# Kernel tuning notes

Hardware: AMD Instinct MI355X
Metric: run time of the kernel (lower is better)

## Reference

```python
import jax, jax.numpy as jnp
import numpy as np

B, QT, KT = 4, 1024, 1024
Q_SIZE, K_SIZE, EMB, HEADS = 1024, 1024, 1024, 8
HEAD_DIM = EMB // HEADS


def setup_inputs() -> dict:
    key = jax.random.key(0)
    ks = jax.random.split(key, 8)
    query = jax.random.normal(ks[0], (B, QT, Q_SIZE), dtype=jnp.float32)
    key_t = jax.random.normal(ks[1], (B, KT, K_SIZE), dtype=jnp.float32)
    mask = jax.random.randint(ks[2], (B, QT, KT), 0, 2, dtype=jnp.int32)
    # Linear weights stored as (in, out); torch Linear computes x @ W.T, equivalent here.
    sq = 1.0 / np.sqrt(Q_SIZE)
    sk = 1.0 / np.sqrt(K_SIZE)
    se = 1.0 / np.sqrt(EMB)
    Wq = jax.random.uniform(ks[3], (Q_SIZE, EMB), jnp.float32, -sq, sq)
    Wk = jax.random.uniform(ks[4], (K_SIZE, EMB), jnp.float32, -sk, sk)
    Wv = jax.random.uniform(ks[5], (K_SIZE, EMB), jnp.float32, -sk, sk)
    Wu = jax.random.uniform(ks[6], (EMB, EMB), jnp.float32, -se, se)
    bu = jax.random.uniform(ks[7], (EMB,), jnp.float32, -se, se)
    return {"query": query, "key": key_t, "mask": mask,
            "Wq": Wq, "Wk": Wk, "Wv": Wv, "Wu": Wu, "bu": bu}


def reference(query, key, mask, Wq, Wk, Wv, Wu, bu):
    b, q_t, _ = query.shape
    k_t = key.shape[1]
    q = (query @ Wq).reshape(b, q_t, HEADS, HEAD_DIM)   # b i n d
    k = (key @ Wk).reshape(b, k_t, HEADS, HEAD_DIM)     # b j n d
    v = (key @ Wv).reshape(b, k_t, HEADS, HEAD_DIM)
    # NOTE: original module defines self.scale but never applies it.
    att_score = jnp.einsum('bind,bjnd->bijn', q, k)
    att_score = jnp.where(mask[..., None] == 0, jnp.float32(-1e9), att_score)
    att_prob = jax.nn.softmax(att_score, axis=2)        # softmax over key axis j
    att_vec = jnp.einsum('bijn,bjnd->bind', att_prob, v).reshape(b, q_t, EMB)
    return att_vec @ Wu + bu
```

## Files before the change

kernel.cpp:

```cpp
#include <hip/hip_runtime.h>
#include <hip/hip_bf16.h>


typedef __attribute__((ext_vector_type(8))) short bf16x8;
typedef __attribute__((ext_vector_type(4))) float f32x4;

static constexpr int BB = 4;
static constexpr int TT = 1024;
static constexpr int EE = 1024;
static constexpr int HH = 8;
static constexpr int DD = 128;

static __device__ __forceinline__ unsigned short f2b(float x) {
  union { float f; unsigned int u; } c; c.f = x;
  unsigned int r = c.u + 0x7fffu + ((c.u >> 16) & 1u);
  return (unsigned short)(r >> 16);
}

static __device__ __forceinline__ unsigned int cvtpk(float lo, float hi) {
  unsigned int r;
  asm("v_cvt_pk_bf16_f32 %0, %1, %2" : "=v"(r) : "v"(lo), "v"(hi));
  return r;
}

static __device__ __forceinline__ void gload_lds16(const void* g, void* l) {
  __builtin_amdgcn_global_load_lds(
      (const __attribute__((address_space(1))) unsigned int*)g,
      (__attribute__((address_space(3))) unsigned int*)l, 16, 0, 0);
}

__global__ __launch_bounds__(256) void cvt_kernel(
    const float* __restrict__ qf, const float* __restrict__ kf,
    unsigned short* __restrict__ qb, unsigned short* __restrict__ kb) {
  int i = blockIdx.x * 256 + threadIdx.x;
  float4 a = ((const float4*)qf)[i];
  ushort4 oa; oa.x = f2b(a.x); oa.y = f2b(a.y); oa.z = f2b(a.z); oa.w = f2b(a.w);
  ((ushort4*)qb)[i] = oa;
  float4 b = ((const float4*)kf)[i];
  ushort4 ob; ob.x = f2b(b.x); ob.y = f2b(b.y); ob.z = f2b(b.z); ob.w = f2b(b.w);
  ((ushort4*)kb)[i] = ob;
}

struct WT4 { const float* src[4]; unsigned short* dst[4]; };

__global__ __launch_bounds__(256) void wtrans_kernel(WT4 wt) {
  const float* src = wt.src[blockIdx.z];
  unsigned short* dst = wt.dst[blockIdx.z];
  __shared__ float tile[32][33];
  int n0 = blockIdx.x * 32, k0 = blockIdx.y * 32;
  int tx = threadIdx.x, ty = threadIdx.y;
#pragma unroll
  for (int i = 0; i < 4; ++i)
    tile[ty + i * 8][tx] = src[(size_t)(k0 + ty + i * 8) * EE + n0 + tx];
  __syncthreads();
#pragma unroll
  for (int i = 0; i < 4; ++i)
    dst[(size_t)(n0 + ty + i * 8) * EE + k0 + tx] = f2b(tile[tx][ty + i * 8]);
}

__global__ __launch_bounds__(256) void vtrans_kernel(
    const unsigned short* __restrict__ vp, unsigned short* __restrict__ vt) {
  int bh = blockIdx.z; int b = bh >> 3, h = bh & 7;
  int d0 = blockIdx.x * 32, kt0 = blockIdx.y * 32;
  __shared__ unsigned short tile[32][33];
  int tx = threadIdx.x, ty = threadIdx.y;
#pragma unroll
  for (int i = 0; i < 4; ++i)
    tile[ty + i * 8][tx] =
        vp[(size_t)(b * TT + kt0 + ty + i * 8) * EE + h * DD + d0 + tx];
  __syncthreads();
#pragma unroll
  for (int i = 0; i < 4; ++i)
    vt[(size_t)((b * HH + h) * DD + d0 + ty + i * 8) * TT + kt0 + tx] =
        tile[tx][ty + i * 8];
}

static __device__ __forceinline__ void gemm_core(
    const unsigned short* __restrict__ A, const unsigned short* __restrict__ Bt,
    unsigned short* __restrict__ Cb, float* __restrict__ Cf,
    const float* __restrict__ bias) {
  constexpr int K = EE, N = EE;
  __shared__ __align__(16) unsigned short As[128 * 32];
  __shared__ __align__(16) unsigned short Bs[128 * 32];
  const int tid = threadIdx.x, lane = tid & 63, w = tid >> 6;
  const int wm = w >> 1, wn = w & 1;
  const int bm = blockIdx.x, bn = blockIdx.y;
  const int g4 = lane >> 4, l15 = lane & 15;
  const int srow = lane >> 2;
  const int scol = (lane & 3) * 8;

  f32x4 acc[4][4] = {};

  for (int kt = 0; kt < K / 32; ++kt) {
    const int k0 = kt * 32;
#pragma unroll
    for (int it = 0; it < 2; ++it) {
      int r = it * 64 + w * 16;
      gload_lds16(A + (size_t)(bm * 128 + r + srow) * K + k0 + scol, As + r * 32);
      gload_lds16(Bt + (size_t)(bn * 128 + r + srow) * K + k0 + scol, Bs + r * 32);
    }
    __syncthreads();
    bf16x8 af[4], bf[4];
#pragma unroll
    for (int i = 0; i < 4; ++i) {
      af[i] = *(const bf16x8*)(As + (wm * 64 + i * 16 + l15) * 32 + g4 * 8);
      bf[i] = *(const bf16x8*)(Bs + (wn * 64 + i * 16 + l15) * 32 + g4 * 8);
    }
#pragma unroll
    for (int i = 0; i < 4; ++i)
#pragma unroll
      for (int j = 0; j < 4; ++j)
        acc[i][j] = __builtin_amdgcn_mfma_f32_16x16x32_bf16(af[i], bf[j],
                                                            acc[i][j], 0, 0, 0);
    __syncthreads();
  }

  const int rr = g4 * 4;
#pragma unroll
  for (int i = 0; i < 4; ++i) {
#pragma unroll
    for (int j = 0; j < 4; ++j) {
      int row = bm * 128 + wm * 64 + i * 16 + rr;
      int col = bn * 128 + wn * 64 + j * 16 + l15;
#pragma unroll
      for (int r = 0; r < 4; ++r) {
        float v = acc[i][j][r];
        if (Cf != nullptr)
          Cf[(size_t)(row + r) * N + col] = v + bias[col];
        else
          Cb[(size_t)(row + r) * N + col] = f2b(v);
      }
    }
  }
}

struct Gemm3 { const unsigned short* A[3]; const unsigned short* Bt[3];
               unsigned short* C[3]; };

__global__ __launch_bounds__(256) void proj_gemm_kernel(Gemm3 g) {
  int z = blockIdx.z;
  gemm_core(g.A[z], g.Bt[z], g.C[z], nullptr, nullptr);
}

__global__ __launch_bounds__(256) void out_gemm_kernel(
    const unsigned short* __restrict__ A, const unsigned short* __restrict__ Bt,
    float* __restrict__ Cf, const float* __restrict__ bias) {
  gemm_core(A, Bt, nullptr, Cf, bias);
}

__global__ __launch_bounds__(256) void attn_kernel(
    const unsigned short* __restrict__ q, const unsigned short* __restrict__ k,
    const unsigned short* __restrict__ vt, const int* __restrict__ mask,
    unsigned short* __restrict__ av) {
  extern __shared__ __align__(16) char smem[];
  unsigned short* Ks = (unsigned short*)smem;
  unsigned short* Vs = (unsigned short*)(smem + 32768);

  const int tid = threadIdx.x, lane = tid & 63, w = tid >> 6;
  const int qt = blockIdx.x, h = blockIdx.y, b = blockIdx.z;
  const int i0 = qt * 64 + w * 16;
  const int g4 = lane >> 4, l15 = lane & 15;

  bf16x8 aq[4];
  {
    const unsigned short* qb =
        q + (size_t)(b * TT + i0 + l15) * EE + h * DD + g4 * 8;
#pragma unroll
    for (int kc = 0; kc < 4; ++kc) aq[kc] = *(const bf16x8*)(qb + kc * 32);
  }

  const unsigned short* kb0 = k + (size_t)(b * TT) * EE + h * DD;
  const unsigned short* vb0 = vt + (size_t)((b * HH + h) * DD) * TT;

  auto stage = [&](int t, int bsel) {
    unsigned short* Kd = Ks + bsel * (64 * 128);
    unsigned short* Vd = Vs + bsel * (128 * 64);
#pragma unroll
    for (int p = 0; p < 4; ++p) {
      int base = p * 256 + w * 64;
      int idx = base + lane;
      int kr = idx >> 4, kc = (idx & 15) ^ (kr & 7);
      gload_lds16(kb0 + (size_t)(t * 64 + kr) * EE + kc * 8, Kd + base * 8);
      int vr = idx >> 3, vc = (idx & 7) ^ (vr & 7);
      gload_lds16(vb0 + (size_t)vr * TT + t * 64 + vc * 8, Vd + base * 8);
    }
  };

  f32x4 oacc[8] = {};
  float mrun = -__builtin_inff(), lrun = 0.f;

  stage(0, 0);
  __syncthreads();
  int buf = 0;

  for (int t = 0; t < 16; ++t) {
    if (t < 15) stage(t + 1, buf ^ 1);

    int4 mreg[4];
    {
      const int* mrow =
          mask + (size_t)(b * TT + i0 + l15) * TT + t * 64 + g4 * 4;
#pragma unroll
      for (int nt = 0; nt < 4; ++nt)
        mreg[nt] = *(const int4*)(mrow + nt * 16);
    }

    const unsigned short* Kb = Ks + buf * 64 * 128;
    const unsigned short* Vb = Vs + buf * 128 * 64;

    f32x4 sacc[4];
    __builtin_amdgcn_s_setprio(1);
#pragma unroll
    for (int nt = 0; nt < 4; ++nt) {
      f32x4 s = {};
#pragma unroll
      for (int kc = 0; kc < 4; ++kc) {
        int krow = nt * 16 + l15;
        int addr = (krow * 256 + (kc * 32 + g4 * 8) * 2) ^ ((krow & 7) << 4);
        bf16x8 bk = *(const bf16x8*)((const char*)Kb + addr);
        s = __builtin_amdgcn_mfma_f32_16x16x32_bf16(bk, aq[kc], s, 0, 0, 0);
      }
      sacc[nt] = s;
    }
    __builtin_amdgcn_s_setprio(0);

#pragma unroll
    for (int nt = 0; nt < 4; ++nt) {
      if (mreg[nt].x == 0) sacc[nt][0] = -1e9f;
      if (mreg[nt].y == 0) sacc[nt][1] = -1e9f;
      if (mreg[nt].z == 0) sacc[nt][2] = -1e9f;
      if (mreg[nt].w == 0) sacc[nt][3] = -1e9f;
    }

    float mx = sacc[0][0];
#pragma unroll
    for (int nt = 0; nt < 4; ++nt)
#pragma unroll
      for (int r = 0; r < 4; ++r) mx = fmaxf(mx, sacc[nt][r]);
    mx = fmaxf(mx, __shfl_xor(mx, 16, 64));
    mx = fmaxf(mx, __shfl_xor(mx, 32, 64));

    if (__any(mx > mrun + 8.f)) {
      float mnew = fmaxf(mrun, mx);
      float sc = __expf(mrun - mnew);
      lrun *= sc;
      mrun = mnew;
      float scO[4];
#pragma unroll
      for (int r = 0; r < 4; ++r)
        scO[r] = __shfl(sc, (lane & 48) | (((lane & 48) >> 2) + r), 64);
#pragma unroll
      for (int dt = 0; dt < 8; ++dt)
#pragma unroll
        for (int r = 0; r < 4; ++r) oacc[dt][r] *= scO[r];
    }

    float p[4][4];
    float s0 = 0.f;
#pragma unroll
    for (int nt = 0; nt < 4; ++nt)
#pragma unroll
      for (int r = 0; r < 4; ++r) {
        float pv = __expf(sacc[nt][r] - mrun);
        p[nt][r] = pv;
        s0 += pv;
      }
    s0 += __shfl_xor(s0, 16, 64);
    s0 += __shfl_xor(s0, 32, 64);
    lrun += s0;

    unsigned int paw[2][4];
#pragma unroll
    for (int h2 = 0; h2 < 2; ++h2) {
      unsigned int D0a = cvtpk(p[2 * h2][0], p[2 * h2][1]);
      unsigned int D1a = cvtpk(p[2 * h2][2], p[2 * h2][3]);
      unsigned int D0b = cvtpk(p[2 * h2 + 1][0], p[2 * h2 + 1][1]);
      unsigned int D1b = cvtpk(p[2 * h2 + 1][2], p[2 * h2 + 1][3]);
      unsigned int r1 = __shfl_xor(g4 < 2 ? D0a : D0b, 16, 64);
      unsigned int r2 = __shfl_xor(g4 < 2 ? D1a : D1b, 16, 64);
      unsigned int r3 = __shfl_xor(g4 == 0 ? D0b : D0a, 32, 64);
      unsigned int r4 = __shfl_xor(g4 == 0 ? D1b : D1a, 32, 64);
      unsigned int r5 = __shfl_xor(g4 == 2 ? D0a : D0b, 48, 64);
      unsigned int r6 = __shfl_xor(g4 == 2 ? D1a : D1b, 48, 64);
      paw[h2][0] = g4 == 0 ? D0a : g4 == 1 ? r5 : g4 == 2 ? r3 : r1;
      paw[h2][1] = g4 == 0 ? D1a : g4 == 1 ? r6 : g4 == 2 ? r4 : r2;
      paw[h2][2] = g4 == 0 ? r1 : g4 == 1 ? r3 : g4 == 2 ? r5 : D0b;
      paw[h2][3] = g4 == 0 ? r2 : g4 == 1 ? r4 : g4 == 2 ? r6 : D1b;
    }

    __builtin_amdgcn_s_setprio(1);
#pragma unroll
    for (int h2 = 0; h2 < 2; ++h2) {
      union { unsigned int u[4]; bf16x8 v; } pau;
      pau.u[0] = paw[h2][0]; pau.u[1] = paw[h2][1];
      pau.u[2] = paw[h2][2]; pau.u[3] = paw[h2][3];
#pragma unroll
      for (int dt = 0; dt < 8; ++dt) {
        int vrow = dt * 16 + l15;
        int addr = (vrow * 128 + (h2 * 32 + g4 * 8) * 2) ^ ((vrow & 7) << 4);
        bf16x8 bv = *(const bf16x8*)((const char*)Vb + addr);
        oacc[dt] = __builtin_amdgcn_mfma_f32_16x16x32_bf16(pau.v, bv, oacc[dt],
                                                           0, 0, 0);
      }
    }
    __builtin_amdgcn_s_setprio(0);

    __syncthreads();
    buf ^= 1;
  }

  float linv[4];
#pragma unroll
  for (int r = 0; r < 4; ++r)
    linv[r] = 1.f / __shfl(lrun, (lane & 48) | (((lane & 48) >> 2) + r), 64);
  unsigned short* ob =
      av + (size_t)(b * TT + i0 + g4 * 4) * EE + h * DD + l15;
#pragma unroll
  for (int dt = 0; dt < 8; ++dt)
#pragma unroll
    for (int r = 0; r < 4; ++r)
      ob[(size_t)r * EE + dt * 16] = f2b(oacc[dt][r] * linv[r]);
}

extern "C" void kernel_launch(void* const* d_in, const int* in_sizes, int n_in,
                              void* d_out, int out_size, void* d_ws,
                              size_t ws_size, hipStream_t stream) {
  const float* query = (const float*)d_in[0];
  const float* key   = (const float*)d_in[1];
  const int*   mask  = (const int*)d_in[2];
  const float* Wq    = (const float*)d_in[3];
  const float* Wk    = (const float*)d_in[4];
  const float* Wv    = (const float*)d_in[5];
  const float* Wu    = (const float*)d_in[6];
  const float* bu    = (const float*)d_in[7];
  float* out = (float*)d_out;

  char* ws = (char*)d_ws;
  const size_t MB = 1024 * 1024;
  unsigned short* qbf = (unsigned short*)(ws);
  unsigned short* kbf = (unsigned short*)(ws + 8 * MB);
  unsigned short* Wqt = (unsigned short*)(ws + 16 * MB);
  unsigned short* Wkt = (unsigned short*)(ws + 18 * MB);
  unsigned short* Wvt = (unsigned short*)(ws + 20 * MB);
  unsigned short* Wut = (unsigned short*)(ws + 22 * MB);
  unsigned short* qp  = (unsigned short*)(ws + 24 * MB);
  unsigned short* kp  = (unsigned short*)(ws + 32 * MB);
  unsigned short* vp  = (unsigned short*)(ws + 40 * MB);
  unsigned short* vtb = (unsigned short*)(ws + 48 * MB);
  unsigned short* av  = (unsigned short*)(ws + 56 * MB);

  cvt_kernel<<<4096, 256, 0, stream>>>(query, key, qbf, kbf);

  WT4 wt; wt.src[0] = Wq; wt.src[1] = Wk; wt.src[2] = Wv; wt.src[3] = Wu;
  wt.dst[0] = Wqt; wt.dst[1] = Wkt; wt.dst[2] = Wvt; wt.dst[3] = Wut;
  wtrans_kernel<<<dim3(32, 32, 4), dim3(32, 8), 0, stream>>>(wt);

  Gemm3 g3;
  g3.A[0] = qbf; g3.A[1] = kbf; g3.A[2] = kbf;
  g3.Bt[0] = Wqt; g3.Bt[1] = Wkt; g3.Bt[2] = Wvt;
  g3.C[0] = qp; g3.C[1] = kp; g3.C[2] = vp;
  proj_gemm_kernel<<<dim3(32, 8, 3), 256, 0, stream>>>(g3);

  vtrans_kernel<<<dim3(4, 32, 32), dim3(32, 8), 0, stream>>>(vp, vtb);

  attn_kernel<<<dim3(16, 8, 4), 256, 65536, stream>>>(qp, kp, vtb, mask, av);

  out_gemm_kernel<<<dim3(32, 8), 256, 0, stream>>>(av, Wut, out, bu);
}
```

Measured before the change: 126.7 us.

## Bit-pack mask, fold log2e into Wq, retile output GEMM, precompute attention addresses

Adds a kernel that packs the int32 mask into 64-bit bitmasks, so the attention kernel reads 1 bit per score instead of 4 bytes from global memory. Scales Wq by log2(e) during the weight transpose so softmax can use raw v_exp_f32 (exp2). Gives the output GEMM its own 64x128 tile, doubling its grid for better CU occupancy. Precomputes the LDS and global addresses in the attention loop and reorders the QK MFMA loop. This adds a kernel launch and reuses the vp workspace region for the mask bits after vtrans has consumed it.

```diff
diff --git a/kernel.cpp b/kernel.cpp
--- a/kernel.cpp
+++ b/kernel.cpp
@@ -20,6 +20,12 @@
 static __device__ __forceinline__ unsigned int cvtpk(float lo, float hi) {
   unsigned int r;
   asm("v_cvt_pk_bf16_f32 %0, %1, %2" : "=v"(r) : "v"(lo), "v"(hi));
+  return r;
+}
+
+static __device__ __forceinline__ float exp2x(float x) {
+  float r;
+  asm("v_exp_f32 %0, %1" : "=v"(r) : "v"(x));
   return r;
 }
 
@@ -41,11 +47,12 @@
   ((ushort4*)kb)[i] = ob;
 }
 
-struct WT4 { const float* src[4]; unsigned short* dst[4]; };
+struct WT4 { const float* src[4]; unsigned short* dst[4]; float scale[4]; };
 
 __global__ __launch_bounds__(256) void wtrans_kernel(WT4 wt) {
   const float* src = wt.src[blockIdx.z];
   unsigned short* dst = wt.dst[blockIdx.z];
+  const float sc = wt.scale[blockIdx.z];
   __shared__ float tile[32][33];
   int n0 = blockIdx.x * 32, k0 = blockIdx.y * 32;
   int tx = threadIdx.x, ty = threadIdx.y;
@@ -55,7 +62,7 @@
   __syncthreads();
 #pragma unroll
   for (int i = 0; i < 4; ++i)
-    dst[(size_t)(n0 + ty + i * 8) * EE + k0 + tx] = f2b(tile[tx][ty + i * 8]);
+    dst[(size_t)(n0 + ty + i * 8) * EE + k0 + tx] = f2b(tile[tx][ty + i * 8] * sc);
 }
 
 __global__ __launch_bounds__(256) void vtrans_kernel(
@@ -75,10 +82,23 @@
         tile[tx][ty + i * 8];
 }
 
+__global__ __launch_bounds__(256) void maskpack_kernel(
+    const int* __restrict__ mask, unsigned long long* __restrict__ mbits) {
+  int row = blockIdx.x * 4 + (threadIdx.x >> 6);
+  int lane = threadIdx.x & 63;
+  const int* mrow = mask + (size_t)row * TT;
+  unsigned long long myw = 0;
+#pragma unroll
+  for (int jw = 0; jw < 16; ++jw) {
+    unsigned long long bal = __ballot(mrow[jw * 64 + lane] != 0);
+    if (lane == jw) myw = bal;
+  }
+  if (lane < 16) mbits[(size_t)row * 16 + lane] = myw;
+}
+
 static __device__ __forceinline__ void gemm_core(
     const unsigned short* __restrict__ A, const unsigned short* __restrict__ Bt,
-    unsigned short* __restrict__ Cb, float* __restrict__ Cf,
-    const float* __restrict__ bias) {
+    unsigned short* __restrict__ Cb) {
   constexpr int K = EE, N = EE;
   __shared__ __align__(16) unsigned short As[128 * 32];
   __shared__ __align__(16) unsigned short Bs[128 * 32];
@@ -117,21 +137,15 @@
 
   const int rr = g4 * 4;
 #pragma unroll
-  for (int i = 0; i < 4; ++i) {
+  for (int i = 0; i < 4; ++i)
 #pragma unroll
     for (int j = 0; j < 4; ++j) {
       int row = bm * 128 + wm * 64 + i * 16 + rr;
       int col = bn * 128 + wn * 64 + j * 16 + l15;
 #pragma unroll
-      for (int r = 0; r < 4; ++r) {
-        float v = acc[i][j][r];
-        if (Cf != nullptr)
-          Cf[(size_t)(row + r) * N + col] = v + bias[col];
-        else
-          Cb[(size_t)(row + r) * N + col] = f2b(v);
-      }
-    }
-  }
+      for (int r = 0; r < 4; ++r)
+        Cb[(size_t)(row + r) * N + col] = f2b(acc[i][j][r]);
+    }
 }
 
 struct Gemm3 { const unsigned short* A[3]; const unsigned short* Bt[3];
@@ -139,27 +153,76 @@
 
 __global__ __launch_bounds__(256) void proj_gemm_kernel(Gemm3 g) {
   int z = blockIdx.z;
-  gemm_core(g.A[z], g.Bt[z], g.C[z], nullptr, nullptr);
+  gemm_core(g.A[z], g.Bt[z], g.C[z]);
 }
 
 __global__ __launch_bounds__(256) void out_gemm_kernel(
     const unsigned short* __restrict__ A, const unsigned short* __restrict__ Bt,
     float* __restrict__ Cf, const float* __restrict__ bias) {
-  gemm_core(A, Bt, nullptr, Cf, bias);
+  constexpr int K = EE, N = EE;
+  __shared__ __align__(16) unsigned short As[64 * 32];
+  __shared__ __align__(16) unsigned short Bs[128 * 32];
+  const int tid = threadIdx.x, lane = tid & 63, w = tid >> 6;
+  const int wm = w >> 1, wn = w & 1;
+  const int bm = blockIdx.x, bn = blockIdx.y;
+  const int g4 = lane >> 4, l15 = lane & 15;
+
+  f32x4 acc[2][4] = {};
+
+  for (int kt = 0; kt < K / 32; ++kt) {
+    const int k0 = kt * 32;
+    {
+      int row = tid >> 2, c = tid & 3;
+      gload_lds16(A + (size_t)(bm * 64 + row) * K + k0 + c * 8, As + tid * 8);
+    }
+#pragma unroll
+    for (int it = 0; it < 2; ++it) {
+      int idx = it * 256 + tid;
+      int row = idx >> 2, c = idx & 3;
+      gload_lds16(Bt + (size_t)(bn * 128 + row) * K + k0 + c * 8, Bs + idx * 8);
+    }
+    __syncthreads();
+    bf16x8 af[2], bf[4];
+#pragma unroll
+    for (int i = 0; i < 2; ++i)
+      af[i] = *(const bf16x8*)(As + (wm * 32 + i * 16 + l15) * 32 + g4 * 8);
+#pragma unroll
+    for (int j = 0; j < 4; ++j)
+      bf[j] = *(const bf16x8*)(Bs + (wn * 64 + j * 16 + l15) * 32 + g4 * 8);
+#pragma unroll
+    for (int i = 0; i < 2; ++i)
+#pragma unroll
+      for (int j = 0; j < 4; ++j)
+        acc[i][j] = __builtin_amdgcn_mfma_f32_16x16x32_bf16(af[i], bf[j],
+                                                            acc[i][j], 0, 0, 0);
+    __syncthreads();
+  }
+
+  const int rr = g4 * 4;
+#pragma unroll
+  for (int i = 0; i < 2; ++i)
+#pragma unroll
+    for (int j = 0; j < 4; ++j) {
+      int row = bm * 64 + wm * 32 + i * 16 + rr;
+      int col = bn * 128 + wn * 64 + j * 16 + l15;
+#pragma unroll
+      for (int r = 0; r < 4; ++r)
+        Cf[(size_t)(row + r) * N + col] = acc[i][j][r] + bias[col];
+    }
 }
 
 __global__ __launch_bounds__(256) void attn_kernel(
     const unsigned short* __restrict__ q, const unsigned short* __restrict__ k,
-    const unsigned short* __restrict__ vt, const int* __restrict__ mask,
+    const unsigned short* __restrict__ vt,
+    const unsigned long long* __restrict__ mbits,
     unsigned short* __restrict__ av) {
   extern __shared__ __align__(16) char smem[];
-  unsigned short* Ks = (unsigned short*)smem;
-  unsigned short* Vs = (unsigned short*)(smem + 32768);
 
   const int tid = threadIdx.x, lane = tid & 63, w = tid >> 6;
   const int qt = blockIdx.x, h = blockIdx.y, b = blockIdx.z;
   const int i0 = qt * 64 + w * 16;
   const int g4 = lane >> 4, l15 = lane & 15;
+  const int swz = (l15 & 7) << 4;
 
   bf16x8 aq[4];
   {
@@ -171,65 +234,81 @@
 
   const unsigned short* kb0 = k + (size_t)(b * TT) * EE + h * DD;
   const unsigned short* vb0 = vt + (size_t)((b * HH + h) * DD) * TT;
-
-  auto stage = [&](int t, int bsel) {
-    unsigned short* Kd = Ks + bsel * (64 * 128);
-    unsigned short* Vd = Vs + bsel * (128 * 64);
-#pragma unroll
-    for (int p = 0; p < 4; ++p) {
-      int base = p * 256 + w * 64;
-      int idx = base + lane;
-      int kr = idx >> 4, kc = (idx & 15) ^ (kr & 7);
-      gload_lds16(kb0 + (size_t)(t * 64 + kr) * EE + kc * 8, Kd + base * 8);
-      int vr = idx >> 3, vc = (idx & 7) ^ (vr & 7);
-      gload_lds16(vb0 + (size_t)vr * TT + t * 64 + vc * 8, Vd + base * 8);
-    }
-  };
+  const unsigned short* kptr[4];
+  const unsigned short* vptr[4];
+  int chunkb[4];
+#pragma unroll
+  for (int p = 0; p < 4; ++p) {
+    int base = p * 256 + w * 64;
+    int idx = base + lane;
+    int kr = idx >> 4, kcc = (idx & 15) ^ (kr & 7);
+    kptr[p] = kb0 + (size_t)kr * EE + kcc * 8;
+    int vr = idx >> 3, vcc = (idx & 7) ^ (vr & 7);
+    vptr[p] = vb0 + (size_t)vr * TT + vcc * 8;
+    chunkb[p] = base * 16;
+  }
+
+  const unsigned long long* mb = mbits + ((size_t)(b * TT + i0 + l15) << 4);
+  unsigned long long mcur = mb[0];
+
+  int kb_[4], vb_[2];
+#pragma unroll
+  for (int kc = 0; kc < 4; ++kc)
+    kb_[kc] = l15 * 256 + ((kc * 64 + g4 * 16) ^ swz);
+#pragma unroll
+  for (int h2 = 0; h2 < 2; ++h2)
+    vb_[h2] = 32768 + l15 * 128 + ((h2 * 64 + g4 * 16) ^ swz);
+
+#pragma unroll
+  for (int p = 0; p < 4; ++p) {
+    gload_lds16(kptr[p], smem + chunkb[p]);
+    gload_lds16(vptr[p], smem + 32768 + chunkb[p]);
+  }
+#pragma unroll
+  for (int p = 0; p < 4; ++p) { kptr[p] += 64 * EE; vptr[p] += 64; }
 
   f32x4 oacc[8] = {};
   float mrun = -__builtin_inff(), lrun = 0.f;
 
-  stage(0, 0);
   __syncthreads();
-  int buf = 0;
+  int bufoff = 0;
 
   for (int t = 0; t < 16; ++t) {
-    if (t < 15) stage(t + 1, buf ^ 1);
-
-    int4 mreg[4];
+    unsigned long long mnext = 0;
+    if (t < 15) {
+      mnext = mb[t + 1];
+      int dst = bufoff ^ 16384;
+#pragma unroll
+      for (int p = 0; p < 4; ++p) {
+        gload_lds16(kptr[p], smem + dst + chunkb[p]);
+        gload_lds16(vptr[p], smem + 32768 + dst + chunkb[p]);
+      }
+#pragma unroll
+      for (int p = 0; p < 4; ++p) { kptr[p] += 64 * EE; vptr[p] += 64; }
+    }
+
+    f32x4 sacc[4] = {};
+    __builtin_amdgcn_s_setprio(1);
+#pragma unroll
+    for (int kc = 0; kc < 4; ++kc)
+#pragma unroll
+      for (int nt = 0; nt < 4; ++nt) {
+        bf16x8 bk = *(const bf16x8*)(smem + kb_[kc] + nt * 4096);
+        sacc[nt] = __builtin_amdgcn_mfma_f32_16x16x32_bf16(bk, aq[kc],
+                                                           sacc[nt], 0, 0, 0);
+      }
+    __builtin_amdgcn_s_setprio(0);
+
     {
-      const int* mrow =
-          mask + (size_t)(b * TT + i0 + l15) * TT + t * 64 + g4 * 4;
-#pragma unroll
-      for (int nt = 0; nt < 4; ++nt)
-        mreg[nt] = *(const int4*)(mrow + nt * 16);
-    }
-
-    const unsigned short* Kb = Ks + buf * 64 * 128;
-    const unsigned short* Vb = Vs + buf * 128 * 64;
-
-    f32x4 sacc[4];
-    __builtin_amdgcn_s_setprio(1);
-#pragma unroll
-    for (int nt = 0; nt < 4; ++nt) {
-      f32x4 s = {};
-#pragma unroll
-      for (int kc = 0; kc < 4; ++kc) {
-        int krow = nt * 16 + l15;
-        int addr = (krow * 256 + (kc * 32 + g4 * 8) * 2) ^ ((krow & 7) << 4);
-        bf16x8 bk = *(const bf16x8*)((const char*)Kb + addr);
-        s = __builtin_amdgcn_mfma_f32_16x16x32_bf16(bk, aq[kc], s, 0, 0, 0);
+      unsigned int wlo = (unsigned int)mcur, whi = (unsigned int)(mcur >> 32);
+#pragma unroll
+      for (int nt = 0; nt < 4; ++nt) {
+        unsigned int ww = (nt < 2) ? wlo : whi;
+        int bb = (nt & 1) * 16 + g4 * 4;
+#pragma unroll
+        for (int r = 0; r < 4; ++r)
+          if (((ww >> (bb + r)) & 1u) == 0u) sacc[nt][r] = -1e9f;
       }
-      sacc[nt] = s;
-    }
-    __builtin_amdgcn_s_setprio(0);
-
-#pragma unroll
-    for (int nt = 0; nt < 4; ++nt) {
-      if (mreg[nt].x == 0) sacc[nt][0] = -1e9f;
-      if (mreg[nt].y == 0) sacc[nt][1] = -1e9f;
-      if (mreg[nt].z == 0) sacc[nt][2] = -1e9f;
-      if (mreg[nt].w == 0) sacc[nt][3] = -1e9f;
     }
 
     float mx = sacc[0][0];
@@ -242,7 +321,7 @@
 
     if (__any(mx > mrun + 8.f)) {
       float mnew = fmaxf(mrun, mx);
-      float sc = __expf(mrun - mnew);
+      float sc = exp2x(mrun - mnew);
       lrun *= sc;
       mrun = mnew;
       float scO[4];
@@ -261,7 +340,7 @@
     for (int nt = 0; nt < 4; ++nt)
 #pragma unroll
       for (int r = 0; r < 4; ++r) {
-        float pv = __expf(sacc[nt][r] - mrun);
+        float pv = exp2x(sacc[nt][r] - mrun);
         p[nt][r] = pv;
         s0 += pv;
       }
@@ -296,9 +375,7 @@
       pau.u[2] = paw[h2][2]; pau.u[3] = paw[h2][3];
 #pragma unroll
       for (int dt = 0; dt < 8; ++dt) {
-        int vrow = dt * 16 + l15;
-        int addr = (vrow * 128 + (h2 * 32 + g4 * 8) * 2) ^ ((vrow & 7) << 4);
-        bf16x8 bv = *(const bf16x8*)((const char*)Vb + addr);
+        bf16x8 bv = *(const bf16x8*)(smem + vb_[h2] + dt * 2048);
         oacc[dt] = __builtin_amdgcn_mfma_f32_16x16x32_bf16(pau.v, bv, oacc[dt],
                                                            0, 0, 0);
       }
@@ -306,7 +383,12 @@
     __builtin_amdgcn_s_setprio(0);
 
     __syncthreads();
-    buf ^= 1;
+    bufoff ^= 16384;
+#pragma unroll
+    for (int kc = 0; kc < 4; ++kc) kb_[kc] ^= 16384;
+#pragma unroll
+    for (int h2 = 0; h2 < 2; ++h2) vb_[h2] ^= 16384;
+    mcur = mnext;
   }
 
   float linv[4];
@@ -348,11 +430,14 @@
   unsigned short* vp  = (unsigned short*)(ws + 40 * MB);
   unsigned short* vtb = (unsigned short*)(ws + 48 * MB);
   unsigned short* av  = (unsigned short*)(ws + 56 * MB);
+  unsigned long long* mbt = (unsigned long long*)(ws + 40 * MB);
 
   cvt_kernel<<<4096, 256, 0, stream>>>(query, key, qbf, kbf);
 
   WT4 wt; wt.src[0] = Wq; wt.src[1] = Wk; wt.src[2] = Wv; wt.src[3] = Wu;
   wt.dst[0] = Wqt; wt.dst[1] = Wkt; wt.dst[2] = Wvt; wt.dst[3] = Wut;
+  wt.scale[0] = 1.4426950408889634f;
+  wt.scale[1] = 1.0f; wt.scale[2] = 1.0f; wt.scale[3] = 1.0f;
   wtrans_kernel<<<dim3(32, 32, 4), dim3(32, 8), 0, stream>>>(wt);
 
   Gemm3 g3;
@@ -363,7 +448,9 @@
 
   vtrans_kernel<<<dim3(4, 32, 32), dim3(32, 8), 0, stream>>>(vp, vtb);
 
-  attn_kernel<<<dim3(16, 8, 4), 256, 65536, stream>>>(qp, kp, vtb, mask, av);
-
-  out_gemm_kernel<<<dim3(32, 8), 256, 0, stream>>>(av, Wut, out, bu);
-}
+  maskpack_kernel<<<1024, 256, 0, stream>>>(mask, mbt);
+
+  attn_kernel<<<dim3(16, 8, 4), 256, 65536, stream>>>(qp, kp, vtb, mbt, av);
+
+  out_gemm_kernel<<<dim3(64, 8), 256, 0, stream>>>(av, Wut, out, bu);
+}
```

After: 119.1 us. 6.0% less time.
